# Optimization experiments

Hardware: AMD Instinct MI355X
Metric: run time of the kernel (lower is better)

## Reference

```python
import jax, jax.numpy as jnp
import numpy as np

B, C, HID, H, W = 4, 256, 128, 64, 64

def setup_inputs() -> dict:
    key = jax.random.key(0)
    k0, k1, k2, k3, k4 = jax.random.split(key, 5)
    x = jax.random.normal(k0, (B, C, H, W), dtype=jnp.float32)
    # 1x1 conv weights, no bias: [out_ch, in_ch]
    s_in = 1.0 / np.sqrt(C)
    s_hid = 1.0 / np.sqrt(HID)
    w_theta = jax.random.uniform(k1, (HID, C), jnp.float32, -s_in, s_in)
    w_phi = jax.random.uniform(k2, (HID, C), jnp.float32, -s_in, s_in)
    w_g = jax.random.uniform(k3, (HID, C), jnp.float32, -s_in, s_in)
    w_mask = jax.random.uniform(k4, (C, HID), jnp.float32, -s_hid, s_hid)
    return {"x": x, "w_theta": w_theta, "w_phi": w_phi, "w_g": w_g, "w_mask": w_mask}

def reference(x, w_theta, w_phi, w_g, w_mask):
    b, c, h, w = x.shape
    n = h * w
    xf = x.reshape(b, c, n)                      # [B,C,N]
    theta = jnp.einsum('oc,bcn->bno', w_theta, xf)  # [B,N,hid]
    phi = jnp.einsum('oc,bcn->bon', w_phi, xf)      # [B,hid,N]
    g = jnp.einsum('oc,bcn->bno', w_g, xf)          # [B,N,hid]
    scores = jnp.einsum('bnk,bkm->bnm', theta, phi)  # [B,N,N], no scale
    attn = jax.nn.softmax(scores, axis=1)            # unconventional axis=1
    out = jnp.einsum('bnm,bmo->bno', attn, g)        # [B,N,hid]
    mask = jnp.einsum('co,bno->bcn', w_mask, out).reshape(b, c, h, w)
    return x + mask
```

## Files before the change

kernel.cpp:

```cpp
#include <hip/hip_runtime.h>

#define BB 4
#define CC 256
#define HIDD 128
#define NN 4096

typedef short s8v __attribute__((ext_vector_type(8)));
typedef _Float16 h8v __attribute__((ext_vector_type(8)));
typedef float f4v __attribute__((ext_vector_type(4)));
typedef unsigned short u16b;

static __device__ __forceinline__ float b2f(unsigned short u) {
    union { unsigned int i; float f; } v; v.i = ((unsigned int)u) << 16; return v.f;
}
static __device__ __forceinline__ unsigned short f2b(float f) {
    union { float f; unsigned int i; } v; v.f = f;
    unsigned int i = v.i;
    return (unsigned short)((i + 0x7fffu + ((i >> 16) & 1u)) >> 16);
}
static __device__ __forceinline__ u16b f2h_bits(float f) {
    union { _Float16 h; u16b u; } v; v.h = (_Float16)f; return v.u;
}

__device__ __forceinline__ int swz(int k, int rc, int CB) {
    return (((k >> 5) * CB + (rc >> 4)) * 64 + ((k >> 3) & 3) * 16 + (rc & 15)) * 8 + (k & 7);
}
__device__ __forceinline__ int gswz(int m, int o) {
    int kb = m >> 5, mm = m & 31;
    int qs = (mm >> 2) & 3;
    int js = ((mm >> 4) & 1) * 4 + (mm & 3);
    return ((kb * 8 + (o >> 4)) * 64 + qs * 16 + (o & 15)) * 8 + js;
}

__global__ __launch_bounds__(256) void prep_kernel(
    const float* __restrict__ wt, const float* __restrict__ wp,
    const float* __restrict__ wg, const float* __restrict__ wm,
    u16b* __restrict__ wF, u16b* __restrict__ wmB)
{
    int t = blockIdx.x * 256 + threadIdx.x;
    wF[t]         = f2h_bits(wt[t]);
    wF[32768 + t] = f2h_bits(wp[t]);
    wF[65536 + t] = f2h_bits(wg[t]);
    wmB[t]        = f2b(wm[t]);
}

__global__ __launch_bounds__(256) void proj_kernel(
    const float* __restrict__ x, const u16b* __restrict__ wF,
    u16b* __restrict__ thetaF, u16b* __restrict__ phiF, u16b* __restrict__ gB)
{
    int wave = blockIdx.x * 4 + (threadIdx.x >> 6);
    int lane = threadIdx.x & 63;
    int l15 = lane & 15, q = lane >> 4;
    int b = wave >> 9;
    int rem = wave & 511;
    int ntile = rem >> 1;
    int half = rem & 1;
    int n0 = ntile << 4;
    const float* xb = x + (size_t)b * CC * NN;

    f4v acc[3][4];
#pragma unroll
    for (int m = 0; m < 3; m++)
#pragma unroll
        for (int i = 0; i < 4; i++) acc[m][i] = (f4v){0.f, 0.f, 0.f, 0.f};

    float xv[8];
    {
        const float* xp = xb + (size_t)(q * 8) * NN + n0 + l15;
#pragma unroll
        for (int j = 0; j < 8; j++) xv[j] = xp[(size_t)j * NN];
    }

    for (int kc = 0; kc < 8; kc++) {
        int c0 = kc * 32;
        float xn[8];
        if (kc < 7) {
            const float* xp = xb + (size_t)(c0 + 32 + q * 8) * NN + n0 + l15;
#pragma unroll
            for (int j = 0; j < 8; j++) xn[j] = xp[(size_t)j * NN];
        }
        h8v bx;
#pragma unroll
        for (int j = 0; j < 8; j++) bx[j] = (_Float16)xv[j];
#pragma unroll
        for (int mat = 0; mat < 3; mat++) {
#pragma unroll
            for (int otl = 0; otl < 4; otl++) {
                int ot = half * 4 + otl;
                const h8v* ap = reinterpret_cast<const h8v*>(
                    wF + mat * 32768 + (ot * 16 + l15) * CC + c0 + q * 8);
                acc[mat][otl] = __builtin_amdgcn_mfma_f32_16x16x32_f16(*ap, bx, acc[mat][otl], 0, 0, 0);
            }
        }
        if (kc < 7) {
#pragma unroll
            for (int j = 0; j < 8; j++) xv[j] = xn[j];
        }
    }

    size_t boff = (size_t)b * (NN * HIDD);
#pragma unroll
    for (int otl = 0; otl < 4; otl++) {
#pragma unroll
        for (int r = 0; r < 4; r++) {
            int o = (half * 4 + otl) * 16 + q * 4 + r;
            int n = n0 + l15;
            int offTP = swz(o, n, NN / 16);
            thetaF[boff + offTP] = f2h_bits(acc[0][otl][r]);
            phiF[boff + offTP]   = f2h_bits(acc[1][otl][r]);
            gB[boff + gswz(n, o)] = f2b(acc[2][otl][r]);
        }
    }
}

__global__ __launch_bounds__(256, 2) void stats_kernel(
    const u16b* __restrict__ thetaF, const u16b* __restrict__ phiF,
    float* __restrict__ Lraw)
{
    int xcd = blockIdx.x & 7;
    int inner = blockIdx.x >> 3;
    int b = xcd >> 1;
    int su = (xcd & 1) * 128 + inner;
    int w = threadIdx.x >> 6;
    int wu = su * 4 + w;
    int mg = wu >> 4;
    int ns = wu & 15;
    int lane = threadIdx.x & 63;

    size_t boff = (size_t)b * (NN * HIDD);
    const u16b* thF = thetaF + boff;
    const u16b* phF = phiF + boff;

    h8v pB[4][4];
#pragma unroll
    for (int mt = 0; mt < 4; mt++)
#pragma unroll
        for (int kb = 0; kb < 4; kb++)
            pB[mt][kb] = *reinterpret_cast<const h8v*>(phF + ((kb * 256 + (mg * 4 + mt)) * 64 + lane) * 8);

    float Lp[4];
#pragma unroll
    for (int i = 0; i < 4; i++) Lp[i] = 0.f;

    for (int i = 0; i < 16; i++) {
        int ntile = ns * 16 + i;
        h8v tA[4];
#pragma unroll
        for (int kb = 0; kb < 4; kb++)
            tA[kb] = *reinterpret_cast<const h8v*>(thF + ((kb * 256 + ntile) * 64 + lane) * 8);
#pragma unroll
        for (int mt = 0; mt < 4; mt++) {
            f4v s = (f4v){0.f, 0.f, 0.f, 0.f};
#pragma unroll
            for (int kb = 0; kb < 4; kb++)
                s = __builtin_amdgcn_mfma_f32_16x16x32_f16(tA[kb], pB[mt][kb], s, 0, 0, 0);
            Lp[mt] += (__expf(s[0]) + __expf(s[1])) + (__expf(s[2]) + __expf(s[3]));
        }
    }
#pragma unroll
    for (int mt = 0; mt < 4; mt++) {
        float v = Lp[mt];
        v += __shfl_xor(v, 16);
        v += __shfl_xor(v, 32);
        if (lane < 16) atomicAdd(&Lraw[b * NN + (mg * 4 + mt) * 16 + lane], v);
    }
}

__global__ __launch_bounds__(256) void rescale_kernel(
    u16b* __restrict__ gB, const float* __restrict__ Lraw)
{
    int t = blockIdx.x * 256 + threadIdx.x;
    int flat0 = t * 8;
    int b = flat0 >> 19;
    int rem = flat0 & ((NN * HIDD) - 1);
    int kb = rem >> 12;
    int lane = (rem >> 3) & 63;
    int qs = lane >> 4;
    int mbase = kb * 32 + qs * 4;
    const float* Lp = Lraw + b * NN + mbase;
    u16b* gp = gB + flat0;
    s8v g = *reinterpret_cast<const s8v*>(gp);
    s8v o;
#pragma unroll
    for (int j = 0; j < 8; j++) {
        float v = b2f((unsigned short)g[j]) / Lp[((j >> 2) << 4) + (j & 3)];
        o[j] = (short)f2b(v);
    }
    *reinterpret_cast<s8v*>(gp) = o;
}

__global__ __launch_bounds__(256, 2) void attn_kernel(
    const u16b* __restrict__ thetaF, const u16b* __restrict__ phiF,
    const u16b* __restrict__ gB, float* __restrict__ outAcc)
{
    int xcd = blockIdx.x & 7;
    int inner = blockIdx.x >> 3;
    int combo = xcd * 4 + (inner & 3);
    int b = combo >> 3;
    int ms = combo & 7;
    int ng = inner >> 2;
    int w = threadIdx.x >> 6;
    int lane = threadIdx.x & 63;
    int l15 = lane & 15, q = lane >> 4;
    int ntile0 = ng * 8 + w * 2;

    size_t boff = (size_t)b * (NN * HIDD);
    const u16b* thF = thetaF + boff;
    const u16b* phF = phiF + boff;
    const u16b* gp = gB + boff;

    h8v tB[2][4];
#pragma unroll
    for (int nt = 0; nt < 2; nt++)
#pragma unroll
        for (int kb = 0; kb < 4; kb++)
            tB[nt][kb] = *reinterpret_cast<const h8v*>(thF + ((kb * 256 + ntile0 + nt) * 64 + lane) * 8);

    f4v acc[2][8];
#pragma unroll
    for (int nt = 0; nt < 2; nt++)
#pragma unroll
        for (int i = 0; i < 8; i++) acc[nt][i] = (f4v){0.f, 0.f, 0.f, 0.f};

    for (int mt = 0; mt < 16; mt++) {
        int m0 = ms * 512 + mt * 32;
        s8v pf[2];
#pragma unroll
        for (int h = 0; h < 2; h++) {
            int mtile = (m0 >> 4) + h;
            h8v pA[4];
#pragma unroll
            for (int kb = 0; kb < 4; kb++)
                pA[kb] = *reinterpret_cast<const h8v*>(phF + ((kb * 256 + mtile) * 64 + lane) * 8);
#pragma unroll
            for (int nt = 0; nt < 2; nt++) {
                f4v s = (f4v){0.f, 0.f, 0.f, 0.f};
#pragma unroll
                for (int kb = 0; kb < 4; kb++)
                    s = __builtin_amdgcn_mfma_f32_16x16x32_f16(pA[kb], tB[nt][kb], s, 0, 0, 0);
#pragma unroll
                for (int r = 0; r < 4; r++)
                    pf[nt][h * 4 + r] = (short)f2b(__expf(s[r]));
            }
        }
        int kb2 = m0 >> 5;
#pragma unroll
        for (int ot = 0; ot < 8; ot++) {
            s8v gf = *reinterpret_cast<const s8v*>(gp + ((kb2 * 8 + ot) * 64 + lane) * 8);
#pragma unroll
            for (int nt = 0; nt < 2; nt++)
                acc[nt][ot] = __builtin_amdgcn_mfma_f32_16x16x32_bf16(pf[nt], gf, acc[nt][ot], 0, 0, 0);
        }
    }

    float* oa = outAcc + (size_t)b * (NN * HIDD);
#pragma unroll
    for (int nt = 0; nt < 2; nt++) {
        int n_base = (ntile0 + nt) * 16;
#pragma unroll
        for (int ot = 0; ot < 8; ot++) {
#pragma unroll
            for (int r = 0; r < 4; r++) {
                int n = n_base + q * 4 + r;
                int o = ot * 16 + l15;
                atomicAdd(&oa[swz(o, n, NN / 16)], acc[nt][ot][r]);
            }
        }
    }
}

__global__ __launch_bounds__(256, 2) void spass_kernel(
    const u16b* __restrict__ thetaF, const u16b* __restrict__ phiF,
    u16b* __restrict__ P, float* __restrict__ Lpart)
{
    int xcd = blockIdx.x & 7;
    int inner = blockIdx.x >> 3;
    int combo = xcd * 8 + (inner & 7);
    int b = combo >> 4;
    int ms = combo & 15;
    int ng = inner >> 3;
    int w = threadIdx.x >> 6;
    int lane = threadIdx.x & 63;
    int l15 = lane & 15, q = lane >> 4;
    int ntile0 = ng * 8 + w * 2;

    size_t boff = (size_t)b * (NN * HIDD);
    const u16b* thF = thetaF + boff;
    const u16b* phF = phiF + boff;
    u16b* Pb = P + (size_t)b * NN * NN;

    __shared__ float Lacc[4][256];

    h8v tB[2][4];
#pragma unroll
    for (int nt = 0; nt < 2; nt++)
#pragma unroll
        for (int kb = 0; kb < 4; kb++)
            tB[nt][kb] = *reinterpret_cast<const h8v*>(thF + ((kb * 256 + ntile0 + nt) * 64 + lane) * 8);

    int ph = ng & 7;
    h8v pA[4];
    {
        int mtile = ms * 16 + ph * 2;
#pragma unroll
        for (int kb = 0; kb < 4; kb++)
            pA[kb] = *reinterpret_cast<const h8v*>(phF + ((kb * 256 + mtile) * 64 + lane) * 8);
    }

    for (int i2 = 0; i2 < 8; i2++) {
        int mtr = (i2 + ph) & 7;
        s8v pf[2];
#pragma unroll
        for (int h = 0; h < 2; h++) {
            int nmtile = (h == 0) ? (ms * 16 + mtr * 2 + 1)
                                  : (ms * 16 + (((i2 + 1 + ph) & 7)) * 2);
            h8v pAN[4];
#pragma unroll
            for (int kb = 0; kb < 4; kb++)
                pAN[kb] = *reinterpret_cast<const h8v*>(phF + ((kb * 256 + nmtile) * 64 + lane) * 8);
            f4v s0 = (f4v){0.f, 0.f, 0.f, 0.f};
            f4v s1 = (f4v){0.f, 0.f, 0.f, 0.f};
#pragma unroll
            for (int kb = 0; kb < 4; kb++) {
                s0 = __builtin_amdgcn_mfma_f32_16x16x32_f16(pA[kb], tB[0][kb], s0, 0, 0, 0);
                s1 = __builtin_amdgcn_mfma_f32_16x16x32_f16(pA[kb], tB[1][kb], s1, 0, 0, 0);
            }
            float ev0[4], ev1[4];
#pragma unroll
            for (int r = 0; r < 4; r++) {
                ev0[r] = __expf(s0[r]);
                ev1[r] = __expf(s1[r]);
            }
#pragma unroll
            for (int r = 0; r < 4; r++) {
                pf[0][h * 4 + r] = (short)f2b(ev0[r]);
                pf[1][h * 4 + r] = (short)f2b(ev1[r]);
            }
            float cs[4];
#pragma unroll
            for (int r = 0; r < 4; r++) {
                cs[r] = ev0[r] + ev1[r];
                cs[r] += __shfl_xor(cs[r], 1);
                cs[r] += __shfl_xor(cs[r], 2);
                cs[r] += __shfl_xor(cs[r], 4);
                cs[r] += __shfl_xor(cs[r], 8);
            }
            if (l15 == 0) {
#pragma unroll
                for (int r = 0; r < 4; r++)
                    Lacc[w][mtr * 32 + h * 16 + q * 4 + r] = cs[r];
            }
#pragma unroll
            for (int kb = 0; kb < 4; kb++) pA[kb] = pAN[kb];
        }
        int kb2 = ms * 8 + mtr;
#pragma unroll
        for (int nt = 0; nt < 2; nt++)
            *reinterpret_cast<s8v*>(
                Pb + ((size_t)(kb2 * 256 + ntile0 + nt) * 64 + lane) * 8) = pf[nt];
    }
    __syncthreads();
    {
        int t = threadIdx.x;
        float s = (Lacc[0][t] + Lacc[1][t]) + (Lacc[2][t] + Lacc[3][t]);
        Lpart[((size_t)(combo * 32 + ng)) * 256 + t] = s;
    }
}

__global__ __launch_bounds__(256) void lrescale_kernel(
    u16b* __restrict__ gB, const float* __restrict__ Lpart)
{
    int t = blockIdx.x;
    int b = t >> 8;
    int kb = (t & 255) >> 1;
    int combo = b * 16 + (kb >> 3);
    int mlbase = (kb & 7) * 32;
    __shared__ float sLp[32][9];
    __shared__ float sL[32];
    int ti = threadIdx.x;
    {
        int mi = ti & 31;
        int ngp = ti >> 5;
        int qs = mi >> 3, h = (mi >> 2) & 1, r = mi & 3;
        int ml = mlbase + qs * 4 + h * 16 + r;
        const float* base = Lpart + ((size_t)(combo * 32 + ngp * 4)) * 256 + ml;
        sLp[mi][ngp] = (base[0] + base[256]) + (base[512] + base[768]);
    }
    __syncthreads();
    if (ti < 32) {
        float s = 0.f;
#pragma unroll
        for (int k = 0; k < 8; k++) s += sLp[ti][k];
        sL[ti] = s;
    }
    __syncthreads();
    size_t flat0 = (size_t)b * (NN * HIDD) + (size_t)(t & 255) * 2048 + (size_t)ti * 8;
    int lane = ti & 63;
    int qs = lane >> 4;
    u16b* gp = gB + flat0;
    s8v g = *reinterpret_cast<const s8v*>(gp);
    s8v o;
#pragma unroll
    for (int j = 0; j < 8; j++) {
        int mi = qs * 8 + ((j >> 2) << 2) + (j & 3);
        float v = b2f((unsigned short)g[j]) / sL[mi];
        o[j] = (short)f2b(v);
    }
    *reinterpret_cast<s8v*>(gp) = o;
}

__global__ __launch_bounds__(256, 4) void pv_kernel(
    const u16b* __restrict__ P, const u16b* __restrict__ gB, u16b* __restrict__ pvPart)
{
    int xcd = blockIdx.x & 7;
    int inner = blockIdx.x >> 3;
    int combo = xcd * 2 + (inner & 1);
    int b = combo >> 2;
    int ms = combo & 3;
    int ng = inner >> 1;
    int w = threadIdx.x >> 6;
    int lane = threadIdx.x & 63;
    int l15 = lane & 15, q = lane >> 4;
    int ntile = ng * 4 + w;

    const u16b* Pb = P + (size_t)b * NN * NN;
    const u16b* gp = gB + (size_t)b * (NN * HIDD);

    f4v acc[8];
#pragma unroll
    for (int i = 0; i < 8; i++) acc[i] = (f4v){0.f, 0.f, 0.f, 0.f};

    int ph = ng & 31;

#define PV_P(it) reinterpret_cast<const s8v*>( \
    Pb + ((size_t)((ms * 32 + (((it) + ph) & 31)) * 256 + ntile) * 64 + lane) * 8)
#define PV_G(it, ot) reinterpret_cast<const s8v*>( \
    gp + (((ms * 32 + (((it) + ph) & 31)) * 8 + (ot)) * 64 + lane) * 8)

    s8v pcur = *PV_P(0);
    s8v pnx  = *PV_P(1);
    s8v ga[8], gb[8];
#pragma unroll
    for (int ot = 0; ot < 8; ot++) ga[ot] = *PV_G(0, ot);
#pragma unroll
    for (int ot = 0; ot < 8; ot++) gb[ot] = *PV_G(1, ot);

    for (int it = 0; it < 32; it += 2) {
        s8v pn2 = *PV_P(it + 2);
#pragma unroll
        for (int ot = 0; ot < 8; ot++)
            acc[ot] = __builtin_amdgcn_mfma_f32_16x16x32_bf16(pcur, ga[ot], acc[ot], 0, 0, 0);
#pragma unroll
        for (int ot = 0; ot < 8; ot++) ga[ot] = *PV_G(it + 2, ot);

        s8v pn3 = *PV_P(it + 3);
#pragma unroll
        for (int ot = 0; ot < 8; ot++)
            acc[ot] = __builtin_amdgcn_mfma_f32_16x16x32_bf16(pnx, gb[ot], acc[ot], 0, 0, 0);
#pragma unroll
        for (int ot = 0; ot < 8; ot++) gb[ot] = *PV_G(it + 3, ot);

        pcur = pn2;
        pnx  = pn3;
    }
#undef PV_P
#undef PV_G

    u16b* pp = pvPart + (size_t)ms * ((size_t)BB * NN * HIDD) + (size_t)b * (NN * HIDD);
    int n_base = ntile * 16;
#pragma unroll
    for (int ot = 0; ot < 8; ot++) {
#pragma unroll
        for (int r = 0; r < 4; r++) {
            int n = n_base + q * 4 + r;
            int o = ot * 16 + l15;
            pp[swz(o, n, NN / 16)] = f2b(acc[ot][r]);
        }
    }
}

__global__ __launch_bounds__(256) void final_big_kernel(
    const float* __restrict__ x, const u16b* __restrict__ wmB,
    const u16b* __restrict__ pvPart, float* __restrict__ y)
{
    int wave = blockIdx.x * 4 + (threadIdx.x >> 6);
    int lane = threadIdx.x & 63;
    int l15 = lane & 15, q = lane >> 4;
    int b = wave >> 10;
    int rem = wave & 1023;
    int ctile = rem >> 6;
    int n64 = rem & 63;
    const size_t pstride = (size_t)BB * NN * HIDD;
    const u16b* pb = pvPart + (size_t)b * (NN * HIDD);
    const float* xb = x + (size_t)b * CC * NN;
    float* yb = y + (size_t)b * CC * NN;
    int c0 = ctile * 16;

    s8v aB[4];
#pragma unroll
    for (int kb = 0; kb < 4; kb++)
        aB[kb] = *reinterpret_cast<const s8v*>(wmB + (c0 + l15) * HIDD + kb * 32 + q * 8);

#pragma unroll
    for (int nt = 0; nt < 4; nt++) {
        int ntile = n64 * 4 + nt;
        f4v acc = (f4v){0.f, 0.f, 0.f, 0.f};
#pragma unroll
        for (int kb = 0; kb < 4; kb++) {
            size_t fo = ((size_t)(kb * 256 + ntile) * 64 + lane) * 8;
            s8v v0 = *reinterpret_cast<const s8v*>(pb + 0 * pstride + fo);
            s8v v1 = *reinterpret_cast<const s8v*>(pb + 1 * pstride + fo);
            s8v v2 = *reinterpret_cast<const s8v*>(pb + 2 * pstride + fo);
            s8v v3 = *reinterpret_cast<const s8v*>(pb + 3 * pstride + fo);
            s8v bv;
#pragma unroll
            for (int j = 0; j < 8; j++) {
                float s = (b2f((unsigned short)v0[j]) + b2f((unsigned short)v1[j]))
                        + (b2f((unsigned short)v2[j]) + b2f((unsigned short)v3[j]));
                bv[j] = (short)f2b(s);
            }
            acc = __builtin_amdgcn_mfma_f32_16x16x32_bf16(aB[kb], bv, acc, 0, 0, 0);
        }
#pragma unroll
        for (int r = 0; r < 4; r++) {
            int c = c0 + q * 4 + r;
            int n = ntile * 16 + l15;
            size_t idx = (size_t)c * NN + n;
            yb[idx] = xb[idx] + acc[r];
        }
    }
}

__global__ __launch_bounds__(256) void final_kernel(
    const float* __restrict__ x, const u16b* __restrict__ wmB,
    const float* __restrict__ outAcc, float* __restrict__ y)
{
    int wave = blockIdx.x * 4 + (threadIdx.x >> 6);
    int lane = threadIdx.x & 63;
    int l15 = lane & 15, q = lane >> 4;
    int b = wave >> 10;
    int rem = wave & 1023;
    int ctile = rem >> 6;
    int n64 = rem & 63;
    const float* oa = outAcc + (size_t)b * (NN * HIDD);
    const float* xb = x + (size_t)b * CC * NN;
    float* yb = y + (size_t)b * CC * NN;
    int c0 = ctile * 16;

    s8v aB[4];
#pragma unroll
    for (int kb = 0; kb < 4; kb++)
        aB[kb] = *reinterpret_cast<const s8v*>(wmB + (c0 + l15) * HIDD + kb * 32 + q * 8);

#pragma unroll
    for (int nt = 0; nt < 4; nt++) {
        int ntile = n64 * 4 + nt;
        f4v acc = (f4v){0.f, 0.f, 0.f, 0.f};
#pragma unroll
        for (int kb = 0; kb < 4; kb++) {
            const float* bp = oa + ((size_t)(kb * 256 + ntile) * 64 + lane) * 8;
            f4v b0 = *reinterpret_cast<const f4v*>(bp);
            f4v b1 = *reinterpret_cast<const f4v*>(bp + 4);
            s8v bv;
#pragma unroll
            for (int j = 0; j < 4; j++) {
                bv[j]     = (short)f2b(b0[j]);
                bv[j + 4] = (short)f2b(b1[j]);
            }
            acc = __builtin_amdgcn_mfma_f32_16x16x32_bf16(aB[kb], bv, acc, 0, 0, 0);
        }
#pragma unroll
        for (int r = 0; r < 4; r++) {
            int c = c0 + q * 4 + r;
            int n = ntile * 16 + l15;
            size_t idx = (size_t)c * NN + n;
            yb[idx] = xb[idx] + acc[r];
        }
    }
}

extern "C" void kernel_launch(void* const* d_in, const int* in_sizes, int n_in,
                              void* d_out, int out_size, void* d_ws, size_t ws_size,
                              hipStream_t stream)
{
    (void)in_sizes; (void)n_in; (void)out_size;
    const float* x  = (const float*)d_in[0];
    const float* wt = (const float*)d_in[1];
    const float* wp = (const float*)d_in[2];
    const float* wg = (const float*)d_in[3];
    const float* wm = (const float*)d_in[4];
    float* y = (float*)d_out;

    char* ws = (char*)d_ws;
    const size_t MB = 1 << 20;
    u16b* thetaF = (u16b*)(ws + 0 * MB);
    u16b* phiF   = (u16b*)(ws + 4 * MB);
    u16b* pvPart = (u16b*)(ws + 0 * MB);
    u16b* gB     = (u16b*)(ws + 16 * MB);
    float* outAcc = (float*)(ws + 20 * MB);
    float* Lraw   = (float*)(ws + 28 * MB);
    char* wbase = ws + 28 * MB + (64 << 10);
    u16b* wF  = (u16b*)(wbase);
    u16b* wmB = (u16b*)(wbase + (192 << 10));
    float* Lpart = (float*)(ws + 30 * MB);
    u16b* P   = (u16b*)(ws + 32 * MB);

    const size_t need_big = 32 * MB + (size_t)BB * NN * NN * sizeof(u16b);
    const bool big = ws_size >= need_big;

    hipLaunchKernelGGL(prep_kernel, dim3(128), dim3(256), 0, stream,
                       wt, wp, wg, wm, wF, wmB);
    hipLaunchKernelGGL(proj_kernel, dim3(512), dim3(256), 0, stream,
                       x, wF, thetaF, phiF, gB);

    if (big) {
        hipLaunchKernelGGL(spass_kernel,    dim3(2048), dim3(256), 0, stream,
                           thetaF, phiF, P, Lpart);
        hipLaunchKernelGGL(lrescale_kernel, dim3(1024), dim3(256), 0, stream, gB, Lpart);
        hipLaunchKernelGGL(pv_kernel,       dim3(1024), dim3(256), 0, stream, P, gB, pvPart);
        hipLaunchKernelGGL(final_big_kernel, dim3(1024), dim3(256), 0, stream,
                           x, wmB, pvPart, y);
    } else {
        hipMemsetAsync(Lraw, 0, (size_t)BB * NN * sizeof(float), stream);
        hipMemsetAsync(outAcc, 0, (size_t)BB * NN * HIDD * sizeof(float), stream);
        hipLaunchKernelGGL(stats_kernel,   dim3(1024), dim3(256), 0, stream,
                           thetaF, phiF, Lraw);
        hipLaunchKernelGGL(rescale_kernel, dim3(1024), dim3(256), 0, stream, gB, Lraw);
        hipLaunchKernelGGL(attn_kernel,    dim3(1024), dim3(256), 0, stream,
                           thetaF, phiF, gB, outAcc);
        hipLaunchKernelGGL(final_kernel,   dim3(1024), dim3(256), 0, stream,
                           x, wmB, outAcc, y);
    }
}
```

Measured before the change: 203.1 us.

## Share g tiles across waves via async global-to-LDS loads in PV kernel

Each of the four waves previously loaded all eight g fragments per k-step from global memory itself. Now each wave issues direct global-to-LDS loads for two of the eight fragments into a 4-slot shared ring, and all waves read the full set from LDS after a barrier. This cuts redundant global/L2 traffic for g by a factor of four. In exchange it adds a block-wide barrier every step, manual vmcnt waits and LDS usage, and lowers the occupancy hint from 4 to 3 blocks per CU.

```diff
diff --git a/kernel.cpp b/kernel.cpp
--- a/kernel.cpp
+++ b/kernel.cpp
@@ -409,7 +409,7 @@
     *reinterpret_cast<s8v*>(gp) = o;
 }
 
-__global__ __launch_bounds__(256, 4) void pv_kernel(
+__global__ __launch_bounds__(256, 3) void pv_kernel(
     const u16b* __restrict__ P, const u16b* __restrict__ gB, u16b* __restrict__ pvPart)
 {
     int xcd = blockIdx.x & 7;
@@ -426,45 +426,65 @@
     const u16b* Pb = P + (size_t)b * NN * NN;
     const u16b* gp = gB + (size_t)b * (NN * HIDD);
 
+    __shared__ __align__(16) u16b gS[4 * 8 * 512];
+
     f4v acc[8];
 #pragma unroll
     for (int i = 0; i < 8; i++) acc[i] = (f4v){0.f, 0.f, 0.f, 0.f};
 
     int ph = ng & 31;
-
-#define PV_P(it) reinterpret_cast<const s8v*>( \
-    Pb + ((size_t)((ms * 32 + (((it) + ph) & 31)) * 256 + ntile) * 64 + lane) * 8)
-#define PV_G(it, ot) reinterpret_cast<const s8v*>( \
-    gp + (((ms * 32 + (((it) + ph) & 31)) * 8 + (ot)) * 64 + lane) * 8)
-
-    s8v pcur = *PV_P(0);
-    s8v pnx  = *PV_P(1);
-    s8v ga[8], gb[8];
-#pragma unroll
-    for (int ot = 0; ot < 8; ot++) ga[ot] = *PV_G(0, ot);
-#pragma unroll
-    for (int ot = 0; ot < 8; ot++) gb[ot] = *PV_G(1, ot);
-
-    for (int it = 0; it < 32; it += 2) {
-        s8v pn2 = *PV_P(it + 2);
-#pragma unroll
-        for (int ot = 0; ot < 8; ot++)
-            acc[ot] = __builtin_amdgcn_mfma_f32_16x16x32_bf16(pcur, ga[ot], acc[ot], 0, 0, 0);
-#pragma unroll
-        for (int ot = 0; ot < 8; ot++) ga[ot] = *PV_G(it + 2, ot);
-
-        s8v pn3 = *PV_P(it + 3);
-#pragma unroll
-        for (int ot = 0; ot < 8; ot++)
-            acc[ot] = __builtin_amdgcn_mfma_f32_16x16x32_bf16(pnx, gb[ot], acc[ot], 0, 0, 0);
-#pragma unroll
-        for (int ot = 0; ot < 8; ot++) gb[ot] = *PV_G(it + 3, ot);
-
-        pcur = pn2;
-        pnx  = pn3;
-    }
-#undef PV_P
-#undef PV_G
+    int ot0 = w * 2;
+
+    s8v p0, p1, p2, p3;
+
+#define PV_KB2(it) (ms * 32 + (((it) + ph) & 31))
+#define PV_ISSUE(it, sl, preg) do {                                              \
+    int kb2_ = PV_KB2(it);                                                       \
+    const u16b* s0_ = gp + (((size_t)(kb2_ * 8 + ot0) * 64 + lane) * 8);         \
+    __builtin_amdgcn_global_load_lds(                                            \
+        (const __attribute__((address_space(1))) unsigned int*)s0_,              \
+        (__attribute__((address_space(3))) unsigned int*)(&gS[((sl) * 8 + ot0) * 512]), \
+        16, 0, 0);                                                               \
+    __builtin_amdgcn_global_load_lds(                                            \
+        (const __attribute__((address_space(1))) unsigned int*)(s0_ + 512),      \
+        (__attribute__((address_space(3))) unsigned int*)(&gS[((sl) * 8 + ot0 + 1) * 512]), \
+        16, 0, 0);                                                               \
+    preg = *reinterpret_cast<const s8v*>(                                        \
+        Pb + ((size_t)(kb2_ * 256 + ntile) * 64 + lane) * 8);                    \
+} while (0)
+
+#define PV_STEP(it, sl, pcons, pnew) do {                                        \
+    PV_ISSUE((it) + 2, ((sl) + 2) & 3, pnew);                                    \
+    __builtin_amdgcn_sched_barrier(0);                                           \
+    asm volatile("s_waitcnt vmcnt(6)" ::: "memory");                             \
+    __builtin_amdgcn_sched_barrier(0);                                           \
+    __builtin_amdgcn_s_barrier();                                                \
+    __builtin_amdgcn_sched_barrier(0);                                           \
+    const s8v* gs_ = reinterpret_cast<const s8v*>(gS) + (sl) * 512 + lane;       \
+    s8v g0_ = gs_[0];   s8v g1_ = gs_[64];  s8v g2_ = gs_[128]; s8v g3_ = gs_[192]; \
+    s8v g4_ = gs_[256]; s8v g5_ = gs_[320]; s8v g6_ = gs_[384]; s8v g7_ = gs_[448]; \
+    acc[0] = __builtin_amdgcn_mfma_f32_16x16x32_bf16(pcons, g0_, acc[0], 0, 0, 0); \
+    acc[1] = __builtin_amdgcn_mfma_f32_16x16x32_bf16(pcons, g1_, acc[1], 0, 0, 0); \
+    acc[2] = __builtin_amdgcn_mfma_f32_16x16x32_bf16(pcons, g2_, acc[2], 0, 0, 0); \
+    acc[3] = __builtin_amdgcn_mfma_f32_16x16x32_bf16(pcons, g3_, acc[3], 0, 0, 0); \
+    acc[4] = __builtin_amdgcn_mfma_f32_16x16x32_bf16(pcons, g4_, acc[4], 0, 0, 0); \
+    acc[5] = __builtin_amdgcn_mfma_f32_16x16x32_bf16(pcons, g5_, acc[5], 0, 0, 0); \
+    acc[6] = __builtin_amdgcn_mfma_f32_16x16x32_bf16(pcons, g6_, acc[6], 0, 0, 0); \
+    acc[7] = __builtin_amdgcn_mfma_f32_16x16x32_bf16(pcons, g7_, acc[7], 0, 0, 0); \
+} while (0)
+
+    PV_ISSUE(0, 0, p0);
+    PV_ISSUE(1, 1, p1);
+
+    for (int i8 = 0; i8 < 32; i8 += 4) {
+        PV_STEP(i8 + 0, 0, p0, p2);
+        PV_STEP(i8 + 1, 1, p1, p3);
+        PV_STEP(i8 + 2, 2, p2, p0);
+        PV_STEP(i8 + 3, 3, p3, p1);
+    }
+#undef PV_STEP
+#undef PV_ISSUE
+#undef PV_KB2
 
     u16b* pp = pvPart + (size_t)ms * ((size_t)BB * NN * HIDD) + (size_t)b * (NN * HIDD);
     int n_base = ntile * 16;
```

New measurement: 182.4 us. 10.2% less time.
